# Optimization experiments

Hardware: AMD Instinct MI355X
Metric: run time of the kernel (lower is better)

The kernel has to match this reference:

```python
import jax, jax.numpy as jnp
import numpy as np

N_DELAYS = 512
N_SAMPLES = 2 ** 15  # 32768


def _interp_linear(x, out_size):
    # F.interpolate(mode='linear', align_corners=False) on [B, C, L]
    L = x.shape[-1]
    scale = L / out_size
    pos = (jnp.arange(out_size, dtype=jnp.float32) + 0.5) * scale - 0.5
    pos = jnp.clip(pos, 0.0, L - 1)
    i0 = jnp.floor(pos).astype(jnp.int32)
    i1 = jnp.minimum(i0 + 1, L - 1)
    w = (pos - i0).astype(x.dtype)
    return x[..., i0] * (1.0 - w) + x[..., i1] * w


def _interp_nearest(x, out_size):
    # F.interpolate(mode='nearest') on [B, C, L]: idx = floor(j * L/out)
    L = x.shape[-1]
    idx = jnp.clip(jnp.floor(jnp.arange(out_size) * (L / out_size)).astype(jnp.int32), 0, L - 1)
    return x[..., idx]


def setup_inputs() -> dict:
    key = jax.random.key(0)
    k1, k2, k3, k4, k5 = jax.random.split(key, 5)
    batch = 8
    impulse = jax.random.normal(k1, (batch, 128), dtype=jnp.float32)
    delay_selection = jax.random.normal(k2, (batch, N_DELAYS, 16), dtype=jnp.float32)
    damping = jax.random.normal(k3, (batch, 1), dtype=jnp.float32)
    filt = jax.random.normal(k4, (batch, 16), dtype=jnp.float32)
    # torch forward draws uniform(-1,1) noise; passed as input for determinism
    noise = jax.random.uniform(k5, (batch, 1, N_SAMPLES), dtype=jnp.float32, minval=-1.0, maxval=1.0)
    # comb-filter buffer: delays[i, ::i+1] = 1
    delays_np = np.zeros((N_DELAYS, N_SAMPLES), dtype=np.float32)
    for i in range(N_DELAYS):
        delays_np[i, ::i + 1] = 1.0
    delays = jnp.asarray(delays_np)
    return {"impulse": impulse, "delay_selection": delay_selection, "damping": damping,
            "filt": filt, "noise": noise, "delays": delays}


def reference(impulse, delay_selection, damping, filt, noise, delays):
    batch = delay_selection.shape[0]
    n_delays, n_samples = delays.shape
    n_frames = filt.shape[-1]

    # filter spectrum envelope: sigmoid -> linear upsample to n_samples//2 -> pad 1
    f = jax.nn.sigmoid(filt).reshape(-1, 1, n_frames)
    f = _interp_linear(f, n_samples // 2)
    filt_spec = jnp.pad(f, ((0, 0), (0, 0), (0, 1)))  # [B,1,n_samples//2+1]

    # impulse: squared envelope upsampled, modulating uniform noise
    imp = impulse.reshape(batch, 1, -1) ** 2
    imp = _interp_linear(imp, n_samples) * noise  # [B,1,n_samples]

    # damping: powers = linspace(1, 1, n_frames) == ones (faithful to source)
    damp = jax.nn.sigmoid(damping.reshape(batch, 1)) * 0.9999
    powers = jnp.linspace(1.0, float(damp.shape[-1]), n_frames)
    damp = damp[:, :, None] ** powers[None, None, :]  # [B,1,n_frames]
    damp = _interp_nearest(damp, n_samples)  # [B,1,n_samples]

    # sparse comb selection: softmax over delays, nearest upsample, weighted sum
    ds = jax.nn.softmax(delay_selection.reshape(batch, n_delays, -1), axis=1)
    ds = _interp_nearest(ds, n_samples)  # [B,n_delays,n_samples]
    d = jnp.einsum('bdn,dn->bn', ds, delays)[:, None, :] * damp  # [B,1,n_samples]

    # FFT convolution
    delay_spec = jnp.fft.rfft(d, axis=-1, norm='ortho')
    impulse_spec = jnp.fft.rfft(imp, axis=-1, norm='ortho')
    spec = delay_spec * impulse_spec * filt_spec
    final = jnp.fft.irfft(spec, n=n_samples, axis=-1, norm='ortho')
    return final
```

## Files before the change

kernel.cpp:

```cpp
#include <hip/hip_runtime.h>
#include <math.h>

#define NSAMP 32768
#define NDEL  512
#define NFR   16
#define BATCH 8
#define TWO_PI 6.283185307179586f

__device__ __forceinline__ float2 cmul(float2 a, float2 b) {
    return make_float2(a.x*b.x - a.y*b.y, a.x*b.y + a.y*b.x);
}
__device__ __forceinline__ float2 cadd(float2 a, float2 b){ return make_float2(a.x+b.x, a.y+b.y); }
__device__ __forceinline__ float2 csub(float2 a, float2 b){ return make_float2(a.x-b.x, a.y-b.y); }
__device__ __forceinline__ float2 crot(float2 z, float sign){ return make_float2(-sign*z.y, sign*z.x); }

__device__ __forceinline__ int phi(int i){ return i + (i >> 3); }

__device__ __forceinline__ void bfly8(const float2 v[8], float sign, float2 X[8]) {
    const float S2 = 0.70710678118654752f;
    float2 t0 = cadd(v[0], v[4]), t1 = csub(v[0], v[4]);
    float2 t2 = cadd(v[2], v[6]), t3 = crot(csub(v[2], v[6]), sign);
    float2 E0 = cadd(t0, t2), E1 = cadd(t1, t3), E2 = csub(t0, t2), E3 = csub(t1, t3);
    float2 u0 = cadd(v[1], v[5]), u1 = csub(v[1], v[5]);
    float2 u2 = cadd(v[3], v[7]), u3 = crot(csub(v[3], v[7]), sign);
    float2 O0 = cadd(u0, u2), O1 = cadd(u1, u3), O2 = csub(u0, u2), O3 = csub(u1, u3);
    float2 c1 = make_float2( S2, sign*S2);
    float2 c3 = make_float2(-S2, sign*S2);
    float2 w1o = cmul(c1, O1);
    float2 w2o = crot(O2, sign);
    float2 w3o = cmul(c3, O3);
    X[0]=cadd(E0,O0);  X[4]=csub(E0,O0);
    X[1]=cadd(E1,w1o); X[5]=csub(E1,w1o);
    X[2]=cadd(E2,w2o); X[6]=csub(E2,w2o);
    X[3]=cadd(E3,w3o); X[7]=csub(E3,w3o);
}

__device__ __forceinline__ void twiddle_q(float2 v[8], float ang1) {
    float sa, ca; __sincosf(ang1, &sa, &ca);
    float2 w1 = make_float2(ca, sa), wq = w1;
#pragma unroll
    for (int q = 1; q < 8; ++q) { v[q] = cmul(v[q], wq); wq = cmul(wq, w1); }
}

__global__ void build_kernel(const float* __restrict__ impulse,
                             const float* __restrict__ dsel,
                             const float* __restrict__ damping,
                             const float* __restrict__ noise,
                             float2* __restrict__ At) {
    const int b   = blockIdx.x >> 6;
    const int f   = (blockIdx.x >> 2) & 15;
    const int sub = blockIdx.x & 3;
    const int tid = threadIdx.x;
    __shared__ float Wrow[NDEL];
    __shared__ float dl[512];

    float v[8], m = -1e30f;
#pragma unroll
    for (int k = 0; k < 8; ++k) {
        v[k] = dsel[(b*NDEL + tid + 64*k)*NFR + f];
        m = fmaxf(m, v[k]);
    }
#pragma unroll
    for (int off = 1; off < 64; off <<= 1) m = fmaxf(m, __shfl_xor(m, off));
    float e[8], s = 0.0f;
#pragma unroll
    for (int k = 0; k < 8; ++k) { e[k] = __expf(v[k] - m); s += e[k]; }
#pragma unroll
    for (int off = 1; off < 64; off <<= 1) s += __shfl_xor(s, off);

    float damp = 1.0f/(1.0f + __expf(-damping[b])) * 0.9999f;
    float scale = damp / s;
#pragma unroll
    for (int k = 0; k < 8; ++k) Wrow[tid + 64*k] = e[k] * scale;
    for (int k = tid; k < 512; k += 64) dl[k] = 0.0f;
    __syncthreads();

    const unsigned start = ((unsigned)f << 11) + ((unsigned)sub << 9);
    const float fstart = (float)start;

    for (unsigned t = 1; t < 64; ++t) {
        float wt = Wrow[t-1];
        unsigned q0 = (unsigned)(__fdividef(fstart, (float)t));
        unsigned n0 = q0 * t;
        while (n0 < start) n0 += t;
        while (n0 >= start + t) n0 -= t;
        for (unsigned i = (n0 - start) + (unsigned)tid * t; i < 512u; i += 64u * t)
            atomicAdd(&dl[i], wt);
    }
    for (unsigned t = 64u + (unsigned)tid; t <= 512u; t += 64u) {
        float wt = Wrow[t-1];
        unsigned q0 = (unsigned)(__fdividef(fstart, (float)t));
        unsigned n0 = q0 * t;
        while (n0 < start) n0 += t;
        while (n0 >= start + t) n0 -= t;
        for (unsigned i = n0 - start; i < 512u; i += t)
            atomicAdd(&dl[i], wt);
    }
    __syncthreads();

    const int n1base = (int)(start >> 6);
    float2* op = At + b*NSAMP + tid*512 + n1base;
#pragma unroll
    for (int q = 0; q < 8; ++q) {
        int n = (int)start + tid + 64*q;
        float pos = (n + 0.5f) * (1.0f/256.0f) - 0.5f;
        pos = fminf(fmaxf(pos, 0.0f), 127.0f);
        int i0 = (int)pos;
        float w = pos - (float)i0;
        int i1 = (i0 + 1 > 127) ? 127 : i0 + 1;
        float x0 = impulse[b*128 + i0]; x0 *= x0;
        float x1 = impulse[b*128 + i1]; x1 *= x1;
        float iv = (x0*(1.0f - w) + x1*w) * noise[b*NSAMP + n];
        op[q] = make_float2(dl[tid + 64*q], iv);
    }
}

__global__ void fft512_fwd_kernel(const float2* __restrict__ src,
                                  float2* __restrict__ dst) {
    const int j  = threadIdx.x;
    const int s  = blockIdx.x >> 6;
    const int n2 = blockIdx.x & 63;
    __shared__ float2 buf[2][576];
    const float sign = -1.0f;

    const float2* sp = src + s * NSAMP;
    float2 v[8], X[8];
#pragma unroll
    for (int q = 0; q < 8; ++q) v[q] = sp[n2*512 + j + 64*q];

    bfly8(v, sign, X);
#pragma unroll
    for (int r = 0; r < 8; ++r) buf[0][phi(8*j + r)] = X[r];
    __syncthreads();
#pragma unroll
    for (int q = 0; q < 8; ++q) v[q] = buf[0][phi(j + 64*q)];
    int jm = j & 7;
    twiddle_q(v, sign * TWO_PI * (float)jm * (1.0f/64.0f));
    bfly8(v, sign, X);
#pragma unroll
    for (int r = 0; r < 8; ++r) buf[1][phi(((j>>3)<<6) + jm + (r<<3))] = X[r];
    __syncthreads();
#pragma unroll
    for (int q = 0; q < 8; ++q) v[q] = buf[1][phi(j + 64*q)];
    twiddle_q(v, sign * TWO_PI * (float)j * (1.0f/512.0f));
    bfly8(v, sign, X);

    float2* dp = dst + s * NSAMP + n2 * 512;
#pragma unroll
    for (int r = 0; r < 8; ++r) {
        int k1 = j + 64*r;
        int pr = (n2 * k1) & (NSAMP - 1);
        float sa, ca; __sincosf(sign * TWO_PI * (float)pr * (1.0f/32768.0f), &sa, &ca);
        dp[k1] = cmul(X[r], make_float2(ca, sa));
    }
}

__global__ void mega_kernel(const float2* __restrict__ G,
                            float2* __restrict__ H,
                            const float* __restrict__ filt) {
    const int l  = threadIdx.x;
    const int cc = l & 7, jj = l >> 3;
    const int s  = blockIdx.x >> 6;
    const int g  = blockIdx.x & 63;
    __shared__ float2 Z[8][65];
    __shared__ float2 buf[576];
    __shared__ float fs[NFR];
    __shared__ int cols[8];

    if (l < NFR) fs[l] = 1.0f/(1.0f + __expf(-filt[s*NFR + l]));
    if (l < 8) {
        int col;
        if (l < 4)        col = 4*g + l;
        else if (g == 0)  col = (l == 4) ? 256 : 512 - (l - 4);
        else              col = 512 - 4*g - (l - 4);
        cols[l] = col;
    }
    __syncthreads();

    const float2* sp = G + s * NSAMP;
    const int mycol = cols[cc];
    float2 v[8], X[8];

#pragma unroll
    for (int q = 0; q < 8; ++q) v[q] = sp[(jj + 8*q)*512 + mycol];
    bfly8(v, -1.0f, X);
#pragma unroll
    for (int r = 0; r < 8; ++r) buf[phi(cc*64 + jj*8 + r)] = X[r];
    __syncthreads();
#pragma unroll
    for (int q = 0; q < 8; ++q) v[q] = buf[phi(cc*64 + jj + 8*q)];
    twiddle_q(v, -TWO_PI * (float)jj * (1.0f/64.0f));
    bfly8(v, -1.0f, X);
#pragma unroll
    for (int r = 0; r < 8; ++r) Z[cc][jj + 8*r] = X[r];
    __syncthreads();

    const float SCALE = 1.0f / (32768.0f * 181.01933598375618f);
#pragma unroll
    for (int it = 0; it < 4; ++it) {
        int c  = l & 3;
        int k2 = (l >> 2) + 16*it;
        if (!(g == 0 && c == 0)) {
            int col = cols[c];
            float2 Zk = Z[c][k2];
            float2 Zr = Z[c+4][63 - k2];
            float2 Zrc = make_float2(Zr.x, -Zr.y);
            float2 D = make_float2(0.5f*(Zk.x + Zrc.x), 0.5f*(Zk.y + Zrc.y));
            float2 df = make_float2(Zk.x - Zrc.x, Zk.y - Zrc.y);
            float2 I = make_float2(0.5f*df.y, -0.5f*df.x);
            int k = col + 512*k2;
            int jjb = (k <= NSAMP - k) ? k : NSAMP - k;
            float fv = 0.0f;
            if (jjb < NSAMP/2) {
                float pos = (jjb + 0.5f) * (1.0f/1024.0f) - 0.5f;
                pos = fminf(fmaxf(pos, 0.0f), 15.0f);
                int i0 = (int)pos;
                float w = pos - (float)i0;
                int i1 = (i0 + 1 > 15) ? 15 : i0 + 1;
                fv = fs[i0]*(1.0f - w) + fs[i1]*w;
            }
            float2 spec = cmul(D, I);
            float gs = fv * SCALE;
            Z[c][k2]        = make_float2( spec.x*gs,  spec.y*gs);
            Z[c+4][63 - k2] = make_float2( spec.x*gs, -spec.y*gs);
        }
    }
    if (g == 0) {
        if (l <= 32) {
            int k2 = l, k2p = (64 - k2) & 63;
            float2 Zk = Z[0][k2];
            float2 Zr = Z[0][k2p];
            float2 Zrc = make_float2(Zr.x, -Zr.y);
            float2 D = make_float2(0.5f*(Zk.x + Zrc.x), 0.5f*(Zk.y + Zrc.y));
            float2 df = make_float2(Zk.x - Zrc.x, Zk.y - Zrc.y);
            float2 I = make_float2(0.5f*df.y, -0.5f*df.x);
            int k = 512*k2;
            int jjb = (k <= NSAMP - k) ? k : NSAMP - k;
            float fv = 0.0f;
            if (jjb < NSAMP/2) {
                float pos = (jjb + 0.5f) * (1.0f/1024.0f) - 0.5f;
                pos = fminf(fmaxf(pos, 0.0f), 15.0f);
                int i0 = (int)pos;
                float w = pos - (float)i0;
                int i1 = (i0 + 1 > 15) ? 15 : i0 + 1;
                fv = fs[i0]*(1.0f - w) + fs[i1]*w;
            }
            float2 spec = cmul(D, I);
            float gs = fv * SCALE;
            Z[0][k2]  = make_float2( spec.x*gs,  spec.y*gs);
            Z[0][k2p] = make_float2( spec.x*gs, -spec.y*gs);
        }
        if (l < 32) {
            int k2 = l, k2p = 63 - k2;
            float2 Zk = Z[4][k2];
            float2 Zr = Z[4][k2p];
            float2 Zrc = make_float2(Zr.x, -Zr.y);
            float2 D = make_float2(0.5f*(Zk.x + Zrc.x), 0.5f*(Zk.y + Zrc.y));
            float2 df = make_float2(Zk.x - Zrc.x, Zk.y - Zrc.y);
            float2 I = make_float2(0.5f*df.y, -0.5f*df.x);
            int k = 256 + 512*k2;
            int jjb = (k <= NSAMP - k) ? k : NSAMP - k;
            float fv = 0.0f;
            {
                float pos = (jjb + 0.5f) * (1.0f/1024.0f) - 0.5f;
                pos = fminf(fmaxf(pos, 0.0f), 15.0f);
                int i0 = (int)pos;
                float w = pos - (float)i0;
                int i1 = (i0 + 1 > 15) ? 15 : i0 + 1;
                fv = fs[i0]*(1.0f - w) + fs[i1]*w;
            }
            float2 spec = cmul(D, I);
            float gs = fv * SCALE;
            Z[4][k2]  = make_float2( spec.x*gs,  spec.y*gs);
            Z[4][k2p] = make_float2( spec.x*gs, -spec.y*gs);
        }
    }
    __syncthreads();

#pragma unroll
    for (int q = 0; q < 8; ++q) v[q] = Z[cc][jj + 8*q];
    bfly8(v, 1.0f, X);
#pragma unroll
    for (int r = 0; r < 8; ++r) buf[phi(cc*64 + jj*8 + r)] = X[r];
    __syncthreads();
#pragma unroll
    for (int q = 0; q < 8; ++q) v[q] = buf[phi(cc*64 + jj + 8*q)];
    twiddle_q(v, TWO_PI * (float)jj * (1.0f/64.0f));
    bfly8(v, 1.0f, X);

    float2* hp = H + s * NSAMP + mycol;
#pragma unroll
    for (int r = 0; r < 8; ++r) {
        int n2 = jj + 8*r;
        int pr = (n2 * mycol) & (NSAMP - 1);
        float sa, ca; __sincosf(TWO_PI * (float)pr * (1.0f/32768.0f), &sa, &ca);
        hp[n2*512] = cmul(X[r], make_float2(ca, sa));
    }
}

__global__ void fft512_out_kernel(const float2* __restrict__ H,
                                  float* __restrict__ out) {
    const int j  = threadIdx.x;
    const int s  = blockIdx.x >> 6;
    const int n2 = blockIdx.x & 63;
    __shared__ float2 buf[2][576];
    const float sign = 1.0f;

    const float2* sp = H + s * NSAMP;
    float2 v[8], X[8];
#pragma unroll
    for (int q = 0; q < 8; ++q) v[q] = sp[n2*512 + j + 64*q];

    bfly8(v, sign, X);
#pragma unroll
    for (int r = 0; r < 8; ++r) buf[0][phi(8*j + r)] = X[r];
    __syncthreads();
#pragma unroll
    for (int q = 0; q < 8; ++q) v[q] = buf[0][phi(j + 64*q)];
    int jm = j & 7;
    twiddle_q(v, sign * TWO_PI * (float)jm * (1.0f/64.0f));
    bfly8(v, sign, X);
#pragma unroll
    for (int r = 0; r < 8; ++r) buf[1][phi(((j>>3)<<6) + jm + (r<<3))] = X[r];
    __syncthreads();
#pragma unroll
    for (int q = 0; q < 8; ++q) v[q] = buf[1][phi(j + 64*q)];
    twiddle_q(v, sign * TWO_PI * (float)j * (1.0f/512.0f));
    bfly8(v, sign, X);

    float* op = out + s * NSAMP + n2;
#pragma unroll
    for (int r = 0; r < 8; ++r) op[64*j + 4096*r] = X[r].x;
}

extern "C" void kernel_launch(void* const* d_in, const int* in_sizes, int n_in,
                              void* d_out, int out_size, void* d_ws, size_t ws_size,
                              hipStream_t stream) {
    const float* impulse = (const float*)d_in[0];
    const float* dsel    = (const float*)d_in[1];
    const float* damping = (const float*)d_in[2];
    const float* filt    = (const float*)d_in[3];
    const float* noise   = (const float*)d_in[4];
    float* out = (float*)d_out;

    float2* A = (float2*)d_ws;
    float2* B = A + BATCH * NSAMP;

    build_kernel     <<<dim3(512), dim3(64), 0, stream>>>(impulse, dsel, damping, noise, A);
    fft512_fwd_kernel<<<dim3(512), dim3(64), 0, stream>>>(A, B);
    mega_kernel      <<<dim3(512), dim3(64), 0, stream>>>(B, A, filt);
    fft512_out_kernel<<<dim3(512), dim3(64), 0, stream>>>(A, out);
}
```

Before: 135.4 us.

## Fuse three FFT convolution kernels into one per-batch block kernel

Replaces the forward FFT, spectrum multiply, and inverse FFT kernels with a single kernel that uses one 1024-thread block per batch element. Each block walks all columns and rows in loops, with thread fences and block barriers between stages instead of separate launches. This removes two kernel launches and the gaps between them. In exchange, parallelism drops from 512 blocks to 8, so only 8 compute units are used, and block-wide syncs are added inside every loop iteration.

```diff
diff --git a/kernel.cpp b/kernel.cpp
--- a/kernel.cpp
+++ b/kernel.cpp
@@ -42,6 +42,12 @@
     for (int q = 1; q < 8; ++q) { v[q] = cmul(v[q], wq); wq = cmul(wq, w1); }
 }
 
+__device__ __forceinline__ int colof(int idx, int g) {
+    if (idx < 4) return 4*g + idx;
+    if (g == 0)  return (idx == 4) ? 256 : 512 - (idx - 4);
+    return 512 - 4*g - (idx - 4);
+}
+
 __global__ void build_kernel(const float* __restrict__ impulse,
                              const float* __restrict__ dsel,
                              const float* __restrict__ damping,
@@ -106,231 +112,235 @@
         float pos = (n + 0.5f) * (1.0f/256.0f) - 0.5f;
         pos = fminf(fmaxf(pos, 0.0f), 127.0f);
         int i0 = (int)pos;
-        float w = pos - (float)i0;
+        float w2 = pos - (float)i0;
         int i1 = (i0 + 1 > 127) ? 127 : i0 + 1;
         float x0 = impulse[b*128 + i0]; x0 *= x0;
         float x1 = impulse[b*128 + i1]; x1 *= x1;
-        float iv = (x0*(1.0f - w) + x1*w) * noise[b*NSAMP + n];
+        float iv = (x0*(1.0f - w2) + x1*w2) * noise[b*NSAMP + n];
         op[q] = make_float2(dl[tid + 64*q], iv);
     }
 }
 
-__global__ void fft512_fwd_kernel(const float2* __restrict__ src,
-                                  float2* __restrict__ dst) {
-    const int j  = threadIdx.x;
-    const int s  = blockIdx.x >> 6;
-    const int n2 = blockIdx.x & 63;
-    __shared__ float2 buf[2][576];
-    const float sign = -1.0f;
-
-    const float2* sp = src + s * NSAMP;
-    float2 v[8], X[8];
-#pragma unroll
-    for (int q = 0; q < 8; ++q) v[q] = sp[n2*512 + j + 64*q];
-
-    bfly8(v, sign, X);
-#pragma unroll
-    for (int r = 0; r < 8; ++r) buf[0][phi(8*j + r)] = X[r];
-    __syncthreads();
-#pragma unroll
-    for (int q = 0; q < 8; ++q) v[q] = buf[0][phi(j + 64*q)];
-    int jm = j & 7;
-    twiddle_q(v, sign * TWO_PI * (float)jm * (1.0f/64.0f));
-    bfly8(v, sign, X);
-#pragma unroll
-    for (int r = 0; r < 8; ++r) buf[1][phi(((j>>3)<<6) + jm + (r<<3))] = X[r];
-    __syncthreads();
-#pragma unroll
-    for (int q = 0; q < 8; ++q) v[q] = buf[1][phi(j + 64*q)];
-    twiddle_q(v, sign * TWO_PI * (float)j * (1.0f/512.0f));
-    bfly8(v, sign, X);
-
-    float2* dp = dst + s * NSAMP + n2 * 512;
-#pragma unroll
-    for (int r = 0; r < 8; ++r) {
-        int k1 = j + 64*r;
-        int pr = (n2 * k1) & (NSAMP - 1);
-        float sa, ca; __sincosf(sign * TWO_PI * (float)pr * (1.0f/32768.0f), &sa, &ca);
-        dp[k1] = cmul(X[r], make_float2(ca, sa));
-    }
-}
-
-__global__ void mega_kernel(const float2* __restrict__ G,
-                            float2* __restrict__ H,
-                            const float* __restrict__ filt) {
-    const int l  = threadIdx.x;
-    const int cc = l & 7, jj = l >> 3;
-    const int s  = blockIdx.x >> 6;
-    const int g  = blockIdx.x & 63;
-    __shared__ float2 Z[8][65];
-    __shared__ float2 buf[576];
-    __shared__ float fs[NFR];
-    __shared__ int cols[8];
-
-    if (l < NFR) fs[l] = 1.0f/(1.0f + __expf(-filt[s*NFR + l]));
-    if (l < 8) {
-        int col;
-        if (l < 4)        col = 4*g + l;
-        else if (g == 0)  col = (l == 4) ? 256 : 512 - (l - 4);
-        else              col = 512 - 4*g - (l - 4);
-        cols[l] = col;
-    }
-    __syncthreads();
-
-    const float2* sp = G + s * NSAMP;
-    const int mycol = cols[cc];
-    float2 v[8], X[8];
-
-#pragma unroll
-    for (int q = 0; q < 8; ++q) v[q] = sp[(jj + 8*q)*512 + mycol];
-    bfly8(v, -1.0f, X);
-#pragma unroll
-    for (int r = 0; r < 8; ++r) buf[phi(cc*64 + jj*8 + r)] = X[r];
-    __syncthreads();
-#pragma unroll
-    for (int q = 0; q < 8; ++q) v[q] = buf[phi(cc*64 + jj + 8*q)];
-    twiddle_q(v, -TWO_PI * (float)jj * (1.0f/64.0f));
-    bfly8(v, -1.0f, X);
-#pragma unroll
-    for (int r = 0; r < 8; ++r) Z[cc][jj + 8*r] = X[r];
-    __syncthreads();
-
-    const float SCALE = 1.0f / (32768.0f * 181.01933598375618f);
-#pragma unroll
-    for (int it = 0; it < 4; ++it) {
-        int c  = l & 3;
-        int k2 = (l >> 2) + 16*it;
-        if (!(g == 0 && c == 0)) {
-            int col = cols[c];
-            float2 Zk = Z[c][k2];
-            float2 Zr = Z[c+4][63 - k2];
-            float2 Zrc = make_float2(Zr.x, -Zr.y);
-            float2 D = make_float2(0.5f*(Zk.x + Zrc.x), 0.5f*(Zk.y + Zrc.y));
-            float2 df = make_float2(Zk.x - Zrc.x, Zk.y - Zrc.y);
-            float2 I = make_float2(0.5f*df.y, -0.5f*df.x);
-            int k = col + 512*k2;
-            int jjb = (k <= NSAMP - k) ? k : NSAMP - k;
-            float fv = 0.0f;
-            if (jjb < NSAMP/2) {
-                float pos = (jjb + 0.5f) * (1.0f/1024.0f) - 0.5f;
-                pos = fminf(fmaxf(pos, 0.0f), 15.0f);
-                int i0 = (int)pos;
-                float w = pos - (float)i0;
-                int i1 = (i0 + 1 > 15) ? 15 : i0 + 1;
-                fv = fs[i0]*(1.0f - w) + fs[i1]*w;
+__global__ void __launch_bounds__(1024) fft_conv_kernel(
+        float2* __restrict__ A,
+        float2* __restrict__ B,
+        const float* __restrict__ filt,
+        float* __restrict__ out) {
+    const int w = threadIdx.x >> 6;
+    const int l = threadIdx.x & 63;
+    const int s = blockIdx.x;
+
+    __shared__ float2 SL[16][1152];
+    __shared__ float fsig[NFR];
+
+    if (threadIdx.x < NFR)
+        fsig[threadIdx.x] = 1.0f/(1.0f + __expf(-filt[s*NFR + threadIdx.x]));
+    __syncthreads();
+
+    {
+        float2* buf0 = &SL[w][0];
+        float2* buf1 = &SL[w][576];
+        const float sign = -1.0f;
+        const float2* sp = A + s * NSAMP;
+        float2* gp = B + s * NSAMP;
+        for (int it = 0; it < 4; ++it) {
+            const int n2 = it * 16 + w;
+            float2 v[8], X[8];
+#pragma unroll
+            for (int q = 0; q < 8; ++q) v[q] = sp[n2*512 + l + 64*q];
+            bfly8(v, sign, X);
+#pragma unroll
+            for (int r = 0; r < 8; ++r) buf0[phi(8*l + r)] = X[r];
+            __syncthreads();
+#pragma unroll
+            for (int q = 0; q < 8; ++q) v[q] = buf0[phi(l + 64*q)];
+            int jm = l & 7;
+            twiddle_q(v, sign * TWO_PI * (float)jm * (1.0f/64.0f));
+            bfly8(v, sign, X);
+#pragma unroll
+            for (int r = 0; r < 8; ++r) buf1[phi(((l>>3)<<6) + jm + (r<<3))] = X[r];
+            __syncthreads();
+#pragma unroll
+            for (int q = 0; q < 8; ++q) v[q] = buf1[phi(l + 64*q)];
+            twiddle_q(v, sign * TWO_PI * (float)l * (1.0f/512.0f));
+            bfly8(v, sign, X);
+
+            float2* dp = gp + n2 * 512;
+#pragma unroll
+            for (int r = 0; r < 8; ++r) {
+                int k1 = l + 64*r;
+                int pr = (n2 * k1) & (NSAMP - 1);
+                float sa, ca; __sincosf(sign * TWO_PI * (float)pr * (1.0f/32768.0f), &sa, &ca);
+                dp[k1] = cmul(X[r], make_float2(ca, sa));
             }
-            float2 spec = cmul(D, I);
-            float gs = fv * SCALE;
-            Z[c][k2]        = make_float2( spec.x*gs,  spec.y*gs);
-            Z[c+4][63 - k2] = make_float2( spec.x*gs, -spec.y*gs);
         }
     }
-    if (g == 0) {
-        if (l <= 32) {
-            int k2 = l, k2p = (64 - k2) & 63;
-            float2 Zk = Z[0][k2];
-            float2 Zr = Z[0][k2p];
-            float2 Zrc = make_float2(Zr.x, -Zr.y);
-            float2 D = make_float2(0.5f*(Zk.x + Zrc.x), 0.5f*(Zk.y + Zrc.y));
-            float2 df = make_float2(Zk.x - Zrc.x, Zk.y - Zrc.y);
-            float2 I = make_float2(0.5f*df.y, -0.5f*df.x);
-            int k = 512*k2;
-            int jjb = (k <= NSAMP - k) ? k : NSAMP - k;
-            float fv = 0.0f;
-            if (jjb < NSAMP/2) {
-                float pos = (jjb + 0.5f) * (1.0f/1024.0f) - 0.5f;
-                pos = fminf(fmaxf(pos, 0.0f), 15.0f);
-                int i0 = (int)pos;
-                float w = pos - (float)i0;
-                int i1 = (i0 + 1 > 15) ? 15 : i0 + 1;
-                fv = fs[i0]*(1.0f - w) + fs[i1]*w;
+    __threadfence();
+    __syncthreads();
+
+    {
+        float2 (*Z)[65] = reinterpret_cast<float2(*)[65]>(&SL[w][0]);
+        float2* mbuf = &SL[w][520];
+        const int cc = l & 7, jj = l >> 3;
+        const float2* sp = B + s * NSAMP;
+        const float SCALE = 1.0f / (32768.0f * 181.01933598375618f);
+
+        for (int it = 0; it < 4; ++it) {
+            const int g = it * 16 + w;
+            const int mycol = colof(cc, g);
+            float2 v[8], X[8];
+
+#pragma unroll
+            for (int q = 0; q < 8; ++q) v[q] = sp[(jj + 8*q)*512 + mycol];
+            bfly8(v, -1.0f, X);
+#pragma unroll
+            for (int r = 0; r < 8; ++r) mbuf[phi(cc*64 + jj*8 + r)] = X[r];
+            __syncthreads();
+#pragma unroll
+            for (int q = 0; q < 8; ++q) v[q] = mbuf[phi(cc*64 + jj + 8*q)];
+            twiddle_q(v, -TWO_PI * (float)jj * (1.0f/64.0f));
+            bfly8(v, -1.0f, X);
+#pragma unroll
+            for (int r = 0; r < 8; ++r) Z[cc][jj + 8*r] = X[r];
+            __syncthreads();
+
+#pragma unroll
+            for (int itp = 0; itp < 4; ++itp) {
+                int c  = l & 3;
+                int k2 = (l >> 2) + 16*itp;
+                if (!(g == 0 && c == 0)) {
+                    int col = colof(c, g);
+                    float2 Zk = Z[c][k2];
+                    float2 Zr = Z[c+4][63 - k2];
+                    float2 Zrc = make_float2(Zr.x, -Zr.y);
+                    float2 D = make_float2(0.5f*(Zk.x + Zrc.x), 0.5f*(Zk.y + Zrc.y));
+                    float2 df = make_float2(Zk.x - Zrc.x, Zk.y - Zrc.y);
+                    float2 I = make_float2(0.5f*df.y, -0.5f*df.x);
+                    int k = col + 512*k2;
+                    int jjb = (k <= NSAMP - k) ? k : NSAMP - k;
+                    float fv = 0.0f;
+                    if (jjb < NSAMP/2) {
+                        float pos = (jjb + 0.5f) * (1.0f/1024.0f) - 0.5f;
+                        pos = fminf(fmaxf(pos, 0.0f), 15.0f);
+                        int i0 = (int)pos;
+                        float w2 = pos - (float)i0;
+                        int i1 = (i0 + 1 > 15) ? 15 : i0 + 1;
+                        fv = fsig[i0]*(1.0f - w2) + fsig[i1]*w2;
+                    }
+                    float2 spec = cmul(D, I);
+                    float gs = fv * SCALE;
+                    Z[c][k2]        = make_float2( spec.x*gs,  spec.y*gs);
+                    Z[c+4][63 - k2] = make_float2( spec.x*gs, -spec.y*gs);
+                }
             }
-            float2 spec = cmul(D, I);
-            float gs = fv * SCALE;
-            Z[0][k2]  = make_float2( spec.x*gs,  spec.y*gs);
-            Z[0][k2p] = make_float2( spec.x*gs, -spec.y*gs);
+            if (g == 0) {
+                if (l <= 32) {
+                    int k2 = l, k2p = (64 - k2) & 63;
+                    float2 Zk = Z[0][k2];
+                    float2 Zr = Z[0][k2p];
+                    float2 Zrc = make_float2(Zr.x, -Zr.y);
+                    float2 D = make_float2(0.5f*(Zk.x + Zrc.x), 0.5f*(Zk.y + Zrc.y));
+                    float2 df = make_float2(Zk.x - Zrc.x, Zk.y - Zrc.y);
+                    float2 I = make_float2(0.5f*df.y, -0.5f*df.x);
+                    int k = 512*k2;
+                    int jjb = (k <= NSAMP - k) ? k : NSAMP - k;
+                    float fv = 0.0f;
+                    if (jjb < NSAMP/2) {
+                        float pos = (jjb + 0.5f) * (1.0f/1024.0f) - 0.5f;
+                        pos = fminf(fmaxf(pos, 0.0f), 15.0f);
+                        int i0 = (int)pos;
+                        float w2 = pos - (float)i0;
+                        int i1 = (i0 + 1 > 15) ? 15 : i0 + 1;
+                        fv = fsig[i0]*(1.0f - w2) + fsig[i1]*w2;
+                    }
+                    float2 spec = cmul(D, I);
+                    float gs = fv * SCALE;
+                    Z[0][k2]  = make_float2( spec.x*gs,  spec.y*gs);
+                    Z[0][k2p] = make_float2( spec.x*gs, -spec.y*gs);
+                }
+                if (l < 32) {
+                    int k2 = l, k2p = 63 - k2;
+                    float2 Zk = Z[4][k2];
+                    float2 Zr = Z[4][k2p];
+                    float2 Zrc = make_float2(Zr.x, -Zr.y);
+                    float2 D = make_float2(0.5f*(Zk.x + Zrc.x), 0.5f*(Zk.y + Zrc.y));
+                    float2 df = make_float2(Zk.x - Zrc.x, Zk.y - Zrc.y);
+                    float2 I = make_float2(0.5f*df.y, -0.5f*df.x);
+                    int k = 256 + 512*k2;
+                    int jjb = (k <= NSAMP - k) ? k : NSAMP - k;
+                    float fv;
+                    {
+                        float pos = (jjb + 0.5f) * (1.0f/1024.0f) - 0.5f;
+                        pos = fminf(fmaxf(pos, 0.0f), 15.0f);
+                        int i0 = (int)pos;
+                        float w2 = pos - (float)i0;
+                        int i1 = (i0 + 1 > 15) ? 15 : i0 + 1;
+                        fv = fsig[i0]*(1.0f - w2) + fsig[i1]*w2;
+                    }
+                    float2 spec = cmul(D, I);
+                    float gs = fv * SCALE;
+                    Z[4][k2]  = make_float2( spec.x*gs,  spec.y*gs);
+                    Z[4][k2p] = make_float2( spec.x*gs, -spec.y*gs);
+                }
+            }
+            __syncthreads();
+
+#pragma unroll
+            for (int q = 0; q < 8; ++q) v[q] = Z[cc][jj + 8*q];
+            bfly8(v, 1.0f, X);
+#pragma unroll
+            for (int r = 0; r < 8; ++r) mbuf[phi(cc*64 + jj*8 + r)] = X[r];
+            __syncthreads();
+#pragma unroll
+            for (int q = 0; q < 8; ++q) v[q] = mbuf[phi(cc*64 + jj + 8*q)];
+            twiddle_q(v, TWO_PI * (float)jj * (1.0f/64.0f));
+            bfly8(v, 1.0f, X);
+
+            float2* hp = A + s * NSAMP + mycol;
+#pragma unroll
+            for (int r = 0; r < 8; ++r) {
+                int n2 = jj + 8*r;
+                int pr = (n2 * mycol) & (NSAMP - 1);
+                float sa, ca; __sincosf(TWO_PI * (float)pr * (1.0f/32768.0f), &sa, &ca);
+                hp[n2*512] = cmul(X[r], make_float2(ca, sa));
+            }
         }
-        if (l < 32) {
-            int k2 = l, k2p = 63 - k2;
-            float2 Zk = Z[4][k2];
-            float2 Zr = Z[4][k2p];
-            float2 Zrc = make_float2(Zr.x, -Zr.y);
-            float2 D = make_float2(0.5f*(Zk.x + Zrc.x), 0.5f*(Zk.y + Zrc.y));
-            float2 df = make_float2(Zk.x - Zrc.x, Zk.y - Zrc.y);
-            float2 I = make_float2(0.5f*df.y, -0.5f*df.x);
-            int k = 256 + 512*k2;
-            int jjb = (k <= NSAMP - k) ? k : NSAMP - k;
-            float fv = 0.0f;
-            {
-                float pos = (jjb + 0.5f) * (1.0f/1024.0f) - 0.5f;
-                pos = fminf(fmaxf(pos, 0.0f), 15.0f);
-                int i0 = (int)pos;
-                float w = pos - (float)i0;
-                int i1 = (i0 + 1 > 15) ? 15 : i0 + 1;
-                fv = fs[i0]*(1.0f - w) + fs[i1]*w;
-            }
-            float2 spec = cmul(D, I);
-            float gs = fv * SCALE;
-            Z[4][k2]  = make_float2( spec.x*gs,  spec.y*gs);
-            Z[4][k2p] = make_float2( spec.x*gs, -spec.y*gs);
+    }
+    __threadfence();
+    __syncthreads();
+
+    {
+        float2* buf0 = &SL[w][0];
+        float2* buf1 = &SL[w][576];
+        const float sign = 1.0f;
+        const float2* sp = A + s * NSAMP;
+        for (int it = 0; it < 4; ++it) {
+            const int n2 = it * 16 + w;
+            float2 v[8], X[8];
+#pragma unroll
+            for (int q = 0; q < 8; ++q) v[q] = sp[n2*512 + l + 64*q];
+            bfly8(v, sign, X);
+#pragma unroll
+            for (int r = 0; r < 8; ++r) buf0[phi(8*l + r)] = X[r];
+            __syncthreads();
+#pragma unroll
+            for (int q = 0; q < 8; ++q) v[q] = buf0[phi(l + 64*q)];
+            int jm = l & 7;
+            twiddle_q(v, sign * TWO_PI * (float)jm * (1.0f/64.0f));
+            bfly8(v, sign, X);
+#pragma unroll
+            for (int r = 0; r < 8; ++r) buf1[phi(((l>>3)<<6) + jm + (r<<3))] = X[r];
+            __syncthreads();
+#pragma unroll
+            for (int q = 0; q < 8; ++q) v[q] = buf1[phi(l + 64*q)];
+            twiddle_q(v, sign * TWO_PI * (float)l * (1.0f/512.0f));
+            bfly8(v, sign, X);
+
+            float* op = out + s * NSAMP + n2;
+#pragma unroll
+            for (int r = 0; r < 8; ++r) op[64*l + 4096*r] = X[r].x;
         }
     }
-    __syncthreads();
-
-#pragma unroll
-    for (int q = 0; q < 8; ++q) v[q] = Z[cc][jj + 8*q];
-    bfly8(v, 1.0f, X);
-#pragma unroll
-    for (int r = 0; r < 8; ++r) buf[phi(cc*64 + jj*8 + r)] = X[r];
-    __syncthreads();
-#pragma unroll
-    for (int q = 0; q < 8; ++q) v[q] = buf[phi(cc*64 + jj + 8*q)];
-    twiddle_q(v, TWO_PI * (float)jj * (1.0f/64.0f));
-    bfly8(v, 1.0f, X);
-
-    float2* hp = H + s * NSAMP + mycol;
-#pragma unroll
-    for (int r = 0; r < 8; ++r) {
-        int n2 = jj + 8*r;
-        int pr = (n2 * mycol) & (NSAMP - 1);
-        float sa, ca; __sincosf(TWO_PI * (float)pr * (1.0f/32768.0f), &sa, &ca);
-        hp[n2*512] = cmul(X[r], make_float2(ca, sa));
-    }
-}
-
-__global__ void fft512_out_kernel(const float2* __restrict__ H,
-                                  float* __restrict__ out) {
-    const int j  = threadIdx.x;
-    const int s  = blockIdx.x >> 6;
-    const int n2 = blockIdx.x & 63;
-    __shared__ float2 buf[2][576];
-    const float sign = 1.0f;
-
-    const float2* sp = H + s * NSAMP;
-    float2 v[8], X[8];
-#pragma unroll
-    for (int q = 0; q < 8; ++q) v[q] = sp[n2*512 + j + 64*q];
-
-    bfly8(v, sign, X);
-#pragma unroll
-    for (int r = 0; r < 8; ++r) buf[0][phi(8*j + r)] = X[r];
-    __syncthreads();
-#pragma unroll
-    for (int q = 0; q < 8; ++q) v[q] = buf[0][phi(j + 64*q)];
-    int jm = j & 7;
-    twiddle_q(v, sign * TWO_PI * (float)jm * (1.0f/64.0f));
-    bfly8(v, sign, X);
-#pragma unroll
-    for (int r = 0; r < 8; ++r) buf[1][phi(((j>>3)<<6) + jm + (r<<3))] = X[r];
-    __syncthreads();
-#pragma unroll
-    for (int q = 0; q < 8; ++q) v[q] = buf[1][phi(j + 64*q)];
-    twiddle_q(v, sign * TWO_PI * (float)j * (1.0f/512.0f));
-    bfly8(v, sign, X);
-
-    float* op = out + s * NSAMP + n2;
-#pragma unroll
-    for (int r = 0; r < 8; ++r) op[64*j + 4096*r] = X[r].x;
 }
 
 extern "C" void kernel_launch(void* const* d_in, const int* in_sizes, int n_in,
@@ -346,8 +356,6 @@
     float2* A = (float2*)d_ws;
     float2* B = A + BATCH * NSAMP;
 
-    build_kernel     <<<dim3(512), dim3(64), 0, stream>>>(impulse, dsel, damping, noise, A);
-    fft512_fwd_kernel<<<dim3(512), dim3(64), 0, stream>>>(A, B);
-    mega_kernel      <<<dim3(512), dim3(64), 0, stream>>>(B, A, filt);
-    fft512_out_kernel<<<dim3(512), dim3(64), 0, stream>>>(A, out);
-}
+    build_kernel   <<<dim3(512), dim3(64),   0, stream>>>(impulse, dsel, damping, noise, A);
+    fft_conv_kernel<<<dim3(BATCH), dim3(1024), 0, stream>>>(A, B, filt, out);
+}
```

Measured after the change: 213.0 us. 1.57x slower.
